# Performance work log

Measured on AMD Instinct MI355X. Metric: run time of the kernel, lower is better.

Reference implementation:

```python
import jax, jax.numpy as jnp
import numpy as np

NUM_BINS = 16

def _compute_histogram(colors, num_bins=NUM_BINS):
    # colors: (N, 3) in [0, 1]
    quantized = (colors * (num_bins - 1)).astype(jnp.int32)
    quantized = jnp.clip(quantized, 0, num_bins - 1)
    # flatten 3D bin index: r*B^2 + g*B + b
    flat_idx = (quantized[:, 0] * num_bins + quantized[:, 1]) * num_bins + quantized[:, 2]
    hist = jax.ops.segment_sum(
        jnp.ones(colors.shape[0], dtype=colors.dtype),
        flat_idx,
        num_segments=num_bins ** 3,
    )
    hist = hist / (hist.sum() + 1e-8)
    return hist  # (num_bins^3,)

def setup_inputs() -> dict:
    key = jax.random.key(0)
    k1, k2 = jax.random.split(key)
    source_colors = jax.random.uniform(k1, (8388608, 3), dtype=jnp.float32)
    target_palette = jax.random.uniform(k2, (4096, 3), dtype=jnp.float32)
    return {"source_colors": source_colors, "target_palette": target_palette}

def reference(source_colors, target_palette):
    source_hist = _compute_histogram(source_colors)
    target_hist = _compute_histogram(target_palette)
    loss = jnp.abs(source_hist - target_hist).mean()
    return loss
```

## Files before the change

### kernel.cpp

```cpp
#include <hip/hip_runtime.h>

#define BINS 4096
#define WORDS 2048
#define H_GRID 1024
#define H_BLOCK 512
#define CHUNKS 16

__device__ __forceinline__ int qz(float c) {
    int q = (int)(c * 15.0f);
    q = q < 0 ? 0 : q;
    q = q > 15 ? 15 : q;
    return q;
}

__device__ __forceinline__ int bin3(float r, float g, float b) {
    return (qz(r) << 8) | (qz(g) << 4) | qz(b);
}

__global__ __launch_bounds__(H_BLOCK, 8) void hist_partial_kernel(
        const float* __restrict__ src, unsigned int* __restrict__ partials,
        int n_pts) {
    __shared__ unsigned int lh[BINS];
    for (int i = threadIdx.x; i < BINS; i += H_BLOCK) lh[i] = 0;
    __syncthreads();

    const float4* __restrict__ src4 = (const float4*)src;
    const int n_quads = n_pts >> 2;
    const int tid = blockIdx.x * H_BLOCK + threadIdx.x;
    const int stride = gridDim.x * H_BLOCK;
    for (int q = tid; q < n_quads; q += stride) {
        float4 a = src4[3 * q + 0];
        float4 b = src4[3 * q + 1];
        float4 c = src4[3 * q + 2];
        atomicAdd(&lh[bin3(a.x, a.y, a.z)], 1u);
        atomicAdd(&lh[bin3(a.w, b.x, b.y)], 1u);
        atomicAdd(&lh[bin3(b.z, b.w, c.x)], 1u);
        atomicAdd(&lh[bin3(c.y, c.z, c.w)], 1u);
    }
    if (blockIdx.x == 0) {
        int tail = n_pts & 3;
        if ((int)threadIdx.x < tail) {
            int p = (n_quads << 2) + threadIdx.x;
            atomicAdd(&lh[bin3(src[3 * p], src[3 * p + 1], src[3 * p + 2])], 1u);
        }
    }
    __syncthreads();

    unsigned int* dst = partials + (size_t)blockIdx.x * WORDS;
#pragma unroll
    for (int p = 0; p < WORDS / H_BLOCK; ++p) {
        int w = threadIdx.x + p * H_BLOCK;
        dst[w] = lh[2 * w] | (lh[2 * w + 1] << 16);
    }
}

__global__ __launch_bounds__(256) void reduce_kernel(
        const unsigned int* __restrict__ partials,
        unsigned int* __restrict__ g_part) {
    const int bin   = (blockIdx.x & 15) * 256 + threadIdx.x;
    const int chunk = blockIdx.x >> 4;
    const int r0    = chunk * (H_GRID / CHUNKS);
    const unsigned short* __restrict__ p16 = (const unsigned short*)partials;
    unsigned int s = 0;
#pragma unroll 16
    for (int r = 0; r < H_GRID / CHUNKS; ++r)
        s += (unsigned int)p16[(size_t)(r0 + r) * BINS + bin];
    g_part[chunk * BINS + bin] = s;
}

__global__ __launch_bounds__(1024) void loss_kernel(
        const float* __restrict__ tgt, const unsigned int* __restrict__ g_part,
        float* __restrict__ out, int n_src, int n_tgt) {
    __shared__ unsigned int th[BINS];
    for (int i = threadIdx.x; i < BINS; i += 1024) th[i] = 0;
    __syncthreads();

    const float4* __restrict__ t4 = (const float4*)tgt;
    const int tq = n_tgt >> 2;
    for (int q = threadIdx.x; q < tq; q += 1024) {
        float4 a = t4[3 * q + 0];
        float4 b = t4[3 * q + 1];
        float4 c = t4[3 * q + 2];
        atomicAdd(&th[bin3(a.x, a.y, a.z)], 1u);
        atomicAdd(&th[bin3(a.w, b.x, b.y)], 1u);
        atomicAdd(&th[bin3(b.z, b.w, c.x)], 1u);
        atomicAdd(&th[bin3(c.y, c.z, c.w)], 1u);
    }
    {
        int tail = n_tgt & 3;
        if ((int)threadIdx.x < tail) {
            int p = (tq << 2) + threadIdx.x;
            atomicAdd(&th[bin3(tgt[3 * p], tgt[3 * p + 1], tgt[3 * p + 2])], 1u);
        }
    }
    __syncthreads();

    const double ns = (double)n_src + 1e-8;
    const double nt = (double)n_tgt + 1e-8;
    double acc = 0.0;
    for (int i = threadIdx.x; i < BINS; i += 1024) {
        unsigned int sv = 0;
#pragma unroll
        for (int c = 0; c < CHUNKS; ++c) sv += g_part[c * BINS + i];
        acc += fabs((double)sv / ns - (double)th[i] / nt);
    }

    for (int off = 32; off > 0; off >>= 1) acc += __shfl_down(acc, off);
    __shared__ double red[16];
    if ((threadIdx.x & 63) == 0) red[threadIdx.x >> 6] = acc;
    __syncthreads();
    if (threadIdx.x == 0) {
        double s = 0.0;
        for (int w = 0; w < 16; ++w) s += red[w];
        out[0] = (float)(s / (double)BINS);
    }
}

extern "C" void kernel_launch(void* const* d_in, const int* in_sizes, int n_in,
                              void* d_out, int out_size, void* d_ws, size_t ws_size,
                              hipStream_t stream) {
    const float* src = (const float*)d_in[0];
    const float* tgt = (const float*)d_in[1];
    const int n_src = in_sizes[0] / 3;
    const int n_tgt = in_sizes[1] / 3;

    unsigned int* partials = (unsigned int*)d_ws;
    unsigned int* g_part   = partials + (size_t)H_GRID * WORDS;

    hist_partial_kernel<<<H_GRID, H_BLOCK, 0, stream>>>(src, partials, n_src);
    reduce_kernel<<<16 * CHUNKS, 256, 0, stream>>>(partials, g_part);
    loss_kernel<<<1, 1024, 0, stream>>>(tgt, g_part, (float*)d_out, n_src, n_tgt);
}
```

Measured before the change: 153.1 us.

## Merge block histograms via global atomics and move target histogram to prep kernel

Drops the partial-histogram buffer and its separate reduce kernel. Each block now atomically adds its nonzero shared-memory bins directly into a global histogram. The target histogram is built in a new single-block prep kernel that also zeroes the global histogram. This leaves the final loss kernel as a plain 4096-bin read. The grid becomes 256 blocks of 1024 threads, and source loads use nontemporal hints. This trades the 8 MB partial write and reread for about a million global atomics contending on 4096 addresses, plus an extra serial single-block launch placed before the main pass.

Measured after the change: 152.5 us. Within noise of the previous version (-0.4%).

```diff
diff --git a/kernel.cpp b/kernel.cpp
--- a/kernel.cpp
+++ b/kernel.cpp
@@ -1,10 +1,10 @@
 #include <hip/hip_runtime.h>
 
 #define BINS 4096
-#define WORDS 2048
-#define H_GRID 1024
-#define H_BLOCK 512
-#define CHUNKS 16
+#define H_GRID 256
+#define H_BLOCK 1024
+
+typedef float f4 __attribute__((ext_vector_type(4)));
 
 __device__ __forceinline__ int qz(float c) {
     int q = (int)(c * 15.0f);
@@ -17,21 +17,53 @@
     return (qz(r) << 8) | (qz(g) << 4) | qz(b);
 }
 
-__global__ __launch_bounds__(H_BLOCK, 8) void hist_partial_kernel(
-        const float* __restrict__ src, unsigned int* __restrict__ partials,
+__global__ __launch_bounds__(1024) void prep_kernel(
+        const float* __restrict__ tgt, unsigned int* __restrict__ g_hist,
+        unsigned int* __restrict__ th, int n_tgt) {
+    __shared__ unsigned int lh[BINS];
+    for (int i = threadIdx.x; i < BINS; i += 1024) {
+        lh[i] = 0;
+        g_hist[i] = 0;
+    }
+    __syncthreads();
+
+    const f4* __restrict__ t4 = (const f4*)tgt;
+    const int tq = n_tgt >> 2;
+    for (int q = threadIdx.x; q < tq; q += 1024) {
+        f4 a = t4[3 * q + 0];
+        f4 b = t4[3 * q + 1];
+        f4 c = t4[3 * q + 2];
+        atomicAdd(&lh[bin3(a.x, a.y, a.z)], 1u);
+        atomicAdd(&lh[bin3(a.w, b.x, b.y)], 1u);
+        atomicAdd(&lh[bin3(b.z, b.w, c.x)], 1u);
+        atomicAdd(&lh[bin3(c.y, c.z, c.w)], 1u);
+    }
+    {
+        int tail = n_tgt & 3;
+        if ((int)threadIdx.x < tail) {
+            int p = (tq << 2) + threadIdx.x;
+            atomicAdd(&lh[bin3(tgt[3 * p], tgt[3 * p + 1], tgt[3 * p + 2])], 1u);
+        }
+    }
+    __syncthreads();
+    for (int i = threadIdx.x; i < BINS; i += 1024) th[i] = lh[i];
+}
+
+__global__ __launch_bounds__(H_BLOCK) void hist_kernel(
+        const float* __restrict__ src, unsigned int* __restrict__ g_hist,
         int n_pts) {
     __shared__ unsigned int lh[BINS];
     for (int i = threadIdx.x; i < BINS; i += H_BLOCK) lh[i] = 0;
     __syncthreads();
 
-    const float4* __restrict__ src4 = (const float4*)src;
+    const f4* __restrict__ src4 = (const f4*)src;
     const int n_quads = n_pts >> 2;
     const int tid = blockIdx.x * H_BLOCK + threadIdx.x;
     const int stride = gridDim.x * H_BLOCK;
     for (int q = tid; q < n_quads; q += stride) {
-        float4 a = src4[3 * q + 0];
-        float4 b = src4[3 * q + 1];
-        float4 c = src4[3 * q + 2];
+        f4 a = __builtin_nontemporal_load(&src4[3 * q + 0]);
+        f4 b = __builtin_nontemporal_load(&src4[3 * q + 1]);
+        f4 c = __builtin_nontemporal_load(&src4[3 * q + 2]);
         atomicAdd(&lh[bin3(a.x, a.y, a.z)], 1u);
         atomicAdd(&lh[bin3(a.w, b.x, b.y)], 1u);
         atomicAdd(&lh[bin3(b.z, b.w, c.x)], 1u);
@@ -46,64 +78,23 @@
     }
     __syncthreads();
 
-    unsigned int* dst = partials + (size_t)blockIdx.x * WORDS;
 #pragma unroll
-    for (int p = 0; p < WORDS / H_BLOCK; ++p) {
-        int w = threadIdx.x + p * H_BLOCK;
-        dst[w] = lh[2 * w] | (lh[2 * w + 1] << 16);
+    for (int p = 0; p < BINS / H_BLOCK; ++p) {
+        int i = threadIdx.x + p * H_BLOCK;
+        unsigned int v = lh[i];
+        if (v) atomicAdd(&g_hist[i], v);
     }
 }
 
-__global__ __launch_bounds__(256) void reduce_kernel(
-        const unsigned int* __restrict__ partials,
-        unsigned int* __restrict__ g_part) {
-    const int bin   = (blockIdx.x & 15) * 256 + threadIdx.x;
-    const int chunk = blockIdx.x >> 4;
-    const int r0    = chunk * (H_GRID / CHUNKS);
-    const unsigned short* __restrict__ p16 = (const unsigned short*)partials;
-    unsigned int s = 0;
-#pragma unroll 16
-    for (int r = 0; r < H_GRID / CHUNKS; ++r)
-        s += (unsigned int)p16[(size_t)(r0 + r) * BINS + bin];
-    g_part[chunk * BINS + bin] = s;
-}
-
 __global__ __launch_bounds__(1024) void loss_kernel(
-        const float* __restrict__ tgt, const unsigned int* __restrict__ g_part,
-        float* __restrict__ out, int n_src, int n_tgt) {
-    __shared__ unsigned int th[BINS];
-    for (int i = threadIdx.x; i < BINS; i += 1024) th[i] = 0;
-    __syncthreads();
-
-    const float4* __restrict__ t4 = (const float4*)tgt;
-    const int tq = n_tgt >> 2;
-    for (int q = threadIdx.x; q < tq; q += 1024) {
-        float4 a = t4[3 * q + 0];
-        float4 b = t4[3 * q + 1];
-        float4 c = t4[3 * q + 2];
-        atomicAdd(&th[bin3(a.x, a.y, a.z)], 1u);
-        atomicAdd(&th[bin3(a.w, b.x, b.y)], 1u);
-        atomicAdd(&th[bin3(b.z, b.w, c.x)], 1u);
-        atomicAdd(&th[bin3(c.y, c.z, c.w)], 1u);
-    }
-    {
-        int tail = n_tgt & 3;
-        if ((int)threadIdx.x < tail) {
-            int p = (tq << 2) + threadIdx.x;
-            atomicAdd(&th[bin3(tgt[3 * p], tgt[3 * p + 1], tgt[3 * p + 2])], 1u);
-        }
-    }
-    __syncthreads();
-
+        const unsigned int* __restrict__ g_hist,
+        const unsigned int* __restrict__ th, float* __restrict__ out,
+        int n_src, int n_tgt) {
     const double ns = (double)n_src + 1e-8;
     const double nt = (double)n_tgt + 1e-8;
     double acc = 0.0;
-    for (int i = threadIdx.x; i < BINS; i += 1024) {
-        unsigned int sv = 0;
-#pragma unroll
-        for (int c = 0; c < CHUNKS; ++c) sv += g_part[c * BINS + i];
-        acc += fabs((double)sv / ns - (double)th[i] / nt);
-    }
+    for (int i = threadIdx.x; i < BINS; i += 1024)
+        acc += fabs((double)g_hist[i] / ns - (double)th[i] / nt);
 
     for (int off = 32; off > 0; off >>= 1) acc += __shfl_down(acc, off);
     __shared__ double red[16];
@@ -124,10 +115,10 @@
     const int n_src = in_sizes[0] / 3;
     const int n_tgt = in_sizes[1] / 3;
 
-    unsigned int* partials = (unsigned int*)d_ws;
-    unsigned int* g_part   = partials + (size_t)H_GRID * WORDS;
+    unsigned int* g_hist = (unsigned int*)d_ws;
+    unsigned int* th     = g_hist + BINS;
 
-    hist_partial_kernel<<<H_GRID, H_BLOCK, 0, stream>>>(src, partials, n_src);
-    reduce_kernel<<<16 * CHUNKS, 256, 0, stream>>>(partials, g_part);
-    loss_kernel<<<1, 1024, 0, stream>>>(tgt, g_part, (float*)d_out, n_src, n_tgt);
+    prep_kernel<<<1, 1024, 0, stream>>>(tgt, g_hist, th, n_tgt);
+    hist_kernel<<<H_GRID, H_BLOCK, 0, stream>>>(src, g_hist, n_src);
+    loss_kernel<<<1, 1024, 0, stream>>>(g_hist, th, (float*)d_out, n_src, n_tgt);
 }
```
